# Performance work log

Measured on AMD Instinct MI355X. Metric: run time of the kernel, lower is better.

Reference implementation:

```python
import jax, jax.numpy as jnp
import numpy as np

IN_DIM = 8
MID = 128
HALF = IN_DIM // 2
N_BLOCKS = 8
B, H, W = 32, 96, 96


def _block_indices():
    # mask/inv_mask 1x1 convs are pure channel selections; precompute index form.
    half = HALF
    a1 = np.arange(half)              # first half channels
    a2 = np.arange(half, IN_DIM)      # second half channels
    b1 = 2 * np.arange(half)          # even channels
    b2 = 2 * np.arange(half) + 1      # odd channels
    # (change_idx, fix_idx) per block, matching self.masks = [(a1,a2),(a2,a1),(b1,b2),(b2,b1)]*2
    return [(a1, a2), (a2, a1), (b1, b2), (b2, b1)] * 2


def setup_inputs() -> dict:
    key = jax.random.key(0)
    ks = jax.random.split(key, 7)
    x = jax.random.normal(ks[0], (B, IN_DIM, H, W), dtype=jnp.float32)
    # stacked per-block 1x1-conv (pointwise) weights of the ST network
    W1 = jax.random.normal(ks[1], (N_BLOCKS, MID, HALF), dtype=jnp.float32) * 0.1
    b1 = jnp.zeros((N_BLOCKS, MID), dtype=jnp.float32)
    W2 = jax.random.normal(ks[2], (N_BLOCKS, MID, MID), dtype=jnp.float32) * 0.05
    b2 = jnp.zeros((N_BLOCKS, MID), dtype=jnp.float32)
    W3 = jax.random.normal(ks[3], (N_BLOCKS, 2 * HALF, MID), dtype=jnp.float32) * 0.05
    b3 = jnp.zeros((N_BLOCKS, 2 * HALF), dtype=jnp.float32)
    return {"x": x, "W1": W1, "b1": b1, "W2": W2, "b2": b2, "W3": W3, "b3": b3}


def _pw(h, w, b):
    # 1x1 conv == channel contraction
    return jnp.einsum('bchw,oc->bohw', h, w) + b[None, :, None, None]


def reference(x, W1, b1, W2, b2, W3, b3):
    pairs = _block_indices()
    log_det = jnp.zeros((x.shape[0], 1, x.shape[2], x.shape[3]), dtype=x.dtype)
    for i, (ci, fi) in enumerate(pairs):
        x_fix = x[:, fi]        # F.conv2d(x, inv_mask): channel gather
        x_change = x[:, ci]     # F.conv2d(x, mask): channel gather
        h = jax.nn.leaky_relu(_pw(x_fix, W1[i], b1[i]), 0.01)
        h = jax.nn.leaky_relu(_pw(h, W2[i], b2[i]), 0.01)
        st = jnp.tanh(_pw(h, W3[i], b3[i]))
        s, t = st[:, :HALF], st[:, HALF:]
        x_change = x_change * jnp.exp(s) + t
        # x*mask_nochange + conv(x_change, mask.T): replace changed channels in place
        x = x.at[:, ci].set(x_change)
        log_det = log_det + s.sum(axis=1, keepdims=True)
    return x, log_det
```

## Files before the change

### kernel.cpp

```cpp
#include <hip/hip_runtime.h>
#include <math.h>
#include <stdint.h>


#define HWPIX   9216
#define NPIX    294912
#define WSTRIDE 45056
#define NFRAG   45
#define L2OFF   4096
#define L3OFF   36864
#define B1OFF   40960
#define B2OFF   41472
#define B3OFF   41984

typedef float    f32x4 __attribute__((ext_vector_type(4)));
typedef _Float16 f16x4 __attribute__((ext_vector_type(4)));
typedef _Float16 f16x8 __attribute__((ext_vector_type(8)));
typedef uint32_t u32x4 __attribute__((ext_vector_type(4)));

__global__ __launch_bounds__(256)
void prep_frags(const float* __restrict__ W1, const float* __restrict__ b1,
                const float* __restrict__ W2, const float* __restrict__ b2,
                const float* __restrict__ W3, const float* __restrict__ b3,
                char* __restrict__ ws)
{
    int t = blockIdx.x * 256 + threadIdx.x;
    if (t >= 8 * NFRAG * 64) return;
    const int lane  = t & 63;
    const int f     = (t >> 6) % NFRAG;
    const int stage = t / (NFRAG * 64);
    const int pl = lane & 15, g = lane >> 4;
    const int pat = stage & 3;
    char* base = ws + stage * WSTRIDE;

    if (f < 8) {
        const int m = f;
        _Float16* dst = (_Float16*)(base + (m >> 1) * 1024 + lane * 16 + (m & 1) * 8);
#pragma unroll
        for (int e = 0; e < 4; ++e) {
            const int k = 4 * g + e;
            float val = 0.f;
            if (k < 8) {
                int j = -1;
                if      (pat == 0) j = (k >= 4) ? (k - 4) : -1;
                else if (pat == 1) j = (k < 4)  ? k        : -1;
                else if (pat == 2) j = (k & 1)  ? (k >> 1) : -1;
                else               j = (k & 1)  ? -1 : (k >> 1);
                if (j >= 0) val = W1[stage * 512 + (16 * m + pl) * 4 + j];
            }
            dst[e] = (_Float16)val;
        }
    } else if (f < 40) {
        const int idx = f - 8, m = idx >> 2, c = idx & 3;
        _Float16* dst = (_Float16*)(base + L2OFF + idx * 1024 + lane * 16);
#pragma unroll
        for (int e = 0; e < 8; ++e) {
            const int k32 = (e < 4) ? (4 * g + e) : (16 + 4 * g + (e - 4));
            dst[e] = (_Float16)W2[stage * 16384 + (16 * m + pl) * 128 + 32 * c + k32];
        }
    } else if (f < 44) {
        const int c = f - 40;
        _Float16* dst = (_Float16*)(base + L3OFF + c * 1024 + lane * 16);
#pragma unroll
        for (int e = 0; e < 8; ++e) {
            const int k32 = (e < 4) ? (4 * g + e) : (16 + 4 * g + (e - 4));
            dst[e] = (pl < 8) ? (_Float16)W3[stage * 1024 + pl * 128 + 32 * c + k32]
                              : (_Float16)0.f;
        }
    } else {
        float* d1 = (float*)(base + B1OFF);
        d1[2 * lane]     = b1[stage * 128 + 2 * lane];
        d1[2 * lane + 1] = b1[stage * 128 + 2 * lane + 1];
        float* d2 = (float*)(base + B2OFF);
        d2[2 * lane]     = b2[stage * 128 + 2 * lane];
        d2[2 * lane + 1] = b2[stage * 128 + 2 * lane + 1];
        if (lane < 16)
            ((float*)(base + B3OFF))[lane] = (lane < 8) ? b3[stage * 8 + lane] : 0.f;
    }
}

__device__ __forceinline__ void load_pair(const void* p, f16x4& a, f16x4& b) {
    f16x8 v = *(const f16x8*)p;
    a = __builtin_shufflevector(v, v, 0, 1, 2, 3);
    b = __builtin_shufflevector(v, v, 4, 5, 6, 7);
}

__device__ __forceinline__ f16x8 cat8(f16x4 a, f16x4 b) {
    return __builtin_shufflevector(a, b, 0, 1, 2, 3, 4, 5, 6, 7);
}

__device__ __forceinline__ f16x4 pack4(float a0, float a1, float a2, float a3) {
    auto lo = __builtin_amdgcn_cvt_pkrtz(a0, a1);
    auto hi = __builtin_amdgcn_cvt_pkrtz(a2, a3);
    f16x4 h;
    h[0] = (_Float16)lo[0]; h[1] = (_Float16)lo[1];
    h[2] = (_Float16)hi[0]; h[3] = (_Float16)hi[1];
    return h;
}

__device__ __forceinline__ f16x4 leaky_cvt(f32x4 a) {
    f16x4 h  = pack4(a[0], a[1], a[2], a[3]);
    f16x4 hs = h * (_Float16)0.01f;
    return __builtin_elementwise_max(h, hs);
}

__device__ __forceinline__ float fast_tanh(float x) {
    float e = __expf(2.0f * x);
    return 1.0f - 2.0f * __builtin_amdgcn_rcpf(e + 1.0f);
}

__global__ __launch_bounds__(256, 3)
void realnvp_mfma(const float* __restrict__ x_in,
                  const char* __restrict__ wfrag,
                  float* __restrict__ out)
{
    __shared__ __align__(16) char lds[WSTRIDE];

    const int tid  = threadIdx.x;
    const int w    = tid >> 6;
    const int lane = tid & 63;
    const int pl = lane & 15, g = lane >> 4;

    const int blockpx = blockIdx.x * 128;
    const int bb   = blockpx / HWPIX;
    const int rem0 = blockpx - bb * HWPIX + w * 32;
    const float* xb = x_in + (size_t)bb * 8 * HWPIX + rem0;

    float xv[2][4];
    float logdet[2] = {0.f, 0.f};
#pragma unroll
    for (int t = 0; t < 2; ++t)
#pragma unroll
        for (int e = 0; e < 4; ++e)
            xv[t][e] = (g < 2) ? xb[(size_t)(4 * g + e) * HWPIX + t * 16 + pl] : 0.f;

#pragma unroll 1
    for (int st = 0; st < 8; ++st) {
        __syncthreads();
        {
            const char* gsrc = wfrag + st * WSTRIDE + tid * 16;
            char*       ldst = lds + tid * 16;
#pragma unroll
            for (int it = 0; it < 11; ++it)
                *(u32x4*)(ldst + it * 4096) = *(const u32x4*)(gsrc + it * 4096);
        }
        __syncthreads();

        f16x4 xh[2];
#pragma unroll
        for (int t = 0; t < 2; ++t)
            xh[t] = pack4(xv[t][0], xv[t][1], xv[t][2], xv[t][3]);

        f16x4 h1[2][8];
        {
            f16x4 w1f[8];
#pragma unroll
            for (int pr = 0; pr < 4; ++pr)
                load_pair(lds + pr * 1024 + lane * 16, w1f[2 * pr], w1f[2 * pr + 1]);
#pragma unroll
            for (int m = 0; m < 8; ++m) {
                f32x4 bv = *(const f32x4*)(lds + B1OFF + m * 64 + g * 16);
#pragma unroll
                for (int t = 0; t < 2; ++t) {
                    f32x4 acc = __builtin_amdgcn_mfma_f32_16x16x16f16(w1f[m], xh[t], bv, 0, 0, 0);
                    h1[t][m] = leaky_cvt(acc);
                }
            }
        }

        f16x4 h2[2][8];
#pragma unroll
        for (int m = 0; m < 8; ++m) {
            f16x8 wf[4];
#pragma unroll
            for (int c = 0; c < 4; ++c)
                wf[c] = *(const f16x8*)(lds + L2OFF + (m * 4 + c) * 1024 + lane * 16);
            f32x4 bv = *(const f32x4*)(lds + B2OFF + m * 64 + g * 16);
#pragma unroll
            for (int t = 0; t < 2; ++t) {
                f32x4 acc = bv;
#pragma unroll
                for (int c = 0; c < 4; ++c)
                    acc = __builtin_amdgcn_mfma_f32_16x16x32_f16(
                        wf[c], cat8(h1[t][2 * c], h1[t][2 * c + 1]), acc, 0, 0, 0);
                h2[t][m] = leaky_cvt(acc);
            }
        }

        {
            f16x8 w3f[4];
#pragma unroll
            for (int c = 0; c < 4; ++c)
                w3f[c] = *(const f16x8*)(lds + L3OFF + c * 1024 + lane * 16);
            f32x4 bv3 = *(const f32x4*)(lds + B3OFF + g * 16);

            const int pat = st & 3;
#pragma unroll
            for (int t = 0; t < 2; ++t) {
                f32x4 acc = bv3;
#pragma unroll
                for (int c = 0; c < 4; ++c)
                    acc = __builtin_amdgcn_mfma_f32_16x16x32_f16(
                        w3f[c], cat8(h2[t][2 * c], h2[t][2 * c + 1]), acc, 0, 0, 0);

                float sv[4], ov[4];
#pragma unroll
                for (int r = 0; r < 4; ++r) sv[r] = fast_tanh(acc[r]);
#pragma unroll
                for (int r = 0; r < 4; ++r)
                    ov[r] = __int_as_float(
                        __builtin_amdgcn_ds_swizzle(__float_as_int(sv[r]), 0x401F));

                if (g == 0) logdet[t] += sv[0] + sv[1] + sv[2] + sv[3];

                float xn[4];
#pragma unroll
                for (int e = 0; e < 4; ++e) xn[e] = xv[t][e];
                if (pat == 0) {
#pragma unroll
                    for (int e = 0; e < 4; ++e)
                        if (g == 0) xn[e] = xv[t][e] * __expf(sv[e]) + ov[e];
                } else if (pat == 1) {
#pragma unroll
                    for (int e = 0; e < 4; ++e)
                        if (g == 1) xn[e] = xv[t][e] * __expf(ov[e]) + sv[e];
                } else if (pat == 2) {
#pragma unroll
                    for (int e = 0; e < 4; e += 2) {
                        const int k0 = e >> 1, k1 = 2 + (e >> 1);
                        if (g == 0) xn[e] = xv[t][e] * __expf(sv[k0]) + ov[k0];
                        if (g == 1) xn[e] = xv[t][e] * __expf(ov[k1]) + sv[k1];
                    }
                } else {
#pragma unroll
                    for (int e = 1; e < 4; e += 2) {
                        const int k0 = e >> 1, k1 = 2 + (e >> 1);
                        if (g == 0) xn[e] = xv[t][e] * __expf(sv[k0]) + ov[k0];
                        if (g == 1) xn[e] = xv[t][e] * __expf(ov[k1]) + sv[k1];
                    }
                }
#pragma unroll
                for (int e = 0; e < 4; ++e) xv[t][e] = xn[e];
            }
        }
    }

    float* outx = out + (size_t)bb * 8 * HWPIX + rem0;
#pragma unroll
    for (int t = 0; t < 2; ++t) {
        if (g < 2)
#pragma unroll
            for (int e = 0; e < 4; ++e)
                outx[(size_t)(4 * g + e) * HWPIX + t * 16 + pl] = xv[t][e];
        if (g == 0)
            out[(size_t)NPIX * 8 + (size_t)bb * HWPIX + rem0 + t * 16 + pl] = logdet[t];
    }
}

extern "C" void kernel_launch(void* const* d_in, const int* in_sizes, int n_in,
                              void* d_out, int out_size, void* d_ws, size_t ws_size,
                              hipStream_t stream)
{
    const float* x  = (const float*)d_in[0];
    const float* W1 = (const float*)d_in[1];
    const float* b1 = (const float*)d_in[2];
    const float* W2 = (const float*)d_in[3];
    const float* b2 = (const float*)d_in[4];
    const float* W3 = (const float*)d_in[5];
    const float* b3 = (const float*)d_in[6];
    float* out = (float*)d_out;
    char*  ws  = (char*)d_ws;

    hipLaunchKernelGGL(prep_frags, dim3(90), dim3(256), 0, stream,
                       W1, b1, W2, b2, W3, b3, ws);
    hipLaunchKernelGGL(realnvp_mfma, dim3(NPIX / 128), dim3(256), 0, stream,
                       x, ws, out);
}
```

Baseline: 175.6 us.

## Prefetch next stage weights into registers and shrink LDS for higher occupancy

Loads the next flow stage's weight fragments from global memory into registers while the current stage computes, then writes them to LDS after a barrier, so the global-load latency overlaps the MFMA work. Biases are now read straight from global memory rather than LDS, which shrinks the LDS buffer to 40 KB, and the launch bound is raised to 4 blocks per CU. The trade-off is 40 extra VGPRs held live across the compute phase, which together with the tighter occupancy target could cause register spills.

```diff
diff --git a/kernel.cpp b/kernel.cpp
--- a/kernel.cpp
+++ b/kernel.cpp
@@ -6,6 +6,7 @@
 #define HWPIX   9216
 #define NPIX    294912
 #define WSTRIDE 45056
+#define LDSBYTES 40960
 #define NFRAG   45
 #define L2OFF   4096
 #define L3OFF   36864
@@ -109,12 +110,12 @@
     return 1.0f - 2.0f * __builtin_amdgcn_rcpf(e + 1.0f);
 }
 
-__global__ __launch_bounds__(256, 3)
+__global__ __launch_bounds__(256, 4)
 void realnvp_mfma(const float* __restrict__ x_in,
                   const char* __restrict__ wfrag,
                   float* __restrict__ out)
 {
-    __shared__ __align__(16) char lds[WSTRIDE];
+    __shared__ __align__(16) char lds[LDSBYTES];
 
     const int tid  = threadIdx.x;
     const int w    = tid >> 6;
@@ -134,17 +135,25 @@
         for (int e = 0; e < 4; ++e)
             xv[t][e] = (g < 2) ? xb[(size_t)(4 * g + e) * HWPIX + t * 16 + pl] : 0.f;
 
+    u32x4 pf[10];
+#pragma unroll
+    for (int it = 0; it < 10; ++it)
+        pf[it] = *(const u32x4*)(wfrag + it * 4096 + tid * 16);
+#pragma unroll
+    for (int it = 0; it < 10; ++it)
+        *(u32x4*)(lds + it * 4096 + tid * 16) = pf[it];
+    __syncthreads();
+
 #pragma unroll 1
     for (int st = 0; st < 8; ++st) {
-        __syncthreads();
-        {
-            const char* gsrc = wfrag + st * WSTRIDE + tid * 16;
-            char*       ldst = lds + tid * 16;
-#pragma unroll
-            for (int it = 0; it < 11; ++it)
-                *(u32x4*)(ldst + it * 4096) = *(const u32x4*)(gsrc + it * 4096);
-        }
-        __syncthreads();
+        if (st < 7) {
+            const char* gsrc = wfrag + (st + 1) * WSTRIDE;
+#pragma unroll
+            for (int it = 0; it < 10; ++it)
+                pf[it] = *(const u32x4*)(gsrc + it * 4096 + tid * 16);
+        }
+
+        const char* bsrc = wfrag + st * WSTRIDE;
 
         f16x4 xh[2];
 #pragma unroll
@@ -159,7 +168,7 @@
                 load_pair(lds + pr * 1024 + lane * 16, w1f[2 * pr], w1f[2 * pr + 1]);
 #pragma unroll
             for (int m = 0; m < 8; ++m) {
-                f32x4 bv = *(const f32x4*)(lds + B1OFF + m * 64 + g * 16);
+                f32x4 bv = *(const f32x4*)(bsrc + B1OFF + m * 64 + g * 16);
 #pragma unroll
                 for (int t = 0; t < 2; ++t) {
                     f32x4 acc = __builtin_amdgcn_mfma_f32_16x16x16f16(w1f[m], xh[t], bv, 0, 0, 0);
@@ -175,7 +184,7 @@
 #pragma unroll
             for (int c = 0; c < 4; ++c)
                 wf[c] = *(const f16x8*)(lds + L2OFF + (m * 4 + c) * 1024 + lane * 16);
-            f32x4 bv = *(const f32x4*)(lds + B2OFF + m * 64 + g * 16);
+            f32x4 bv = *(const f32x4*)(bsrc + B2OFF + m * 64 + g * 16);
 #pragma unroll
             for (int t = 0; t < 2; ++t) {
                 f32x4 acc = bv;
@@ -192,7 +201,7 @@
 #pragma unroll
             for (int c = 0; c < 4; ++c)
                 w3f[c] = *(const f16x8*)(lds + L3OFF + c * 1024 + lane * 16);
-            f32x4 bv3 = *(const f32x4*)(lds + B3OFF + g * 16);
+            f32x4 bv3 = *(const f32x4*)(bsrc + B3OFF + g * 16);
 
             const int pat = st & 3;
 #pragma unroll
@@ -243,6 +252,14 @@
                 for (int e = 0; e < 4; ++e) xv[t][e] = xn[e];
             }
         }
+
+        __syncthreads();
+        if (st < 7) {
+#pragma unroll
+            for (int it = 0; it < 10; ++it)
+                *(u32x4*)(lds + it * 4096 + tid * 16) = pf[it];
+        }
+        __syncthreads();
     }
 
     float* outx = out + (size_t)bb * 8 * HWPIX + rem0;
```

Result: slower. 316.4 us (+80.1%).

## Process four pixel tiles per wave and read biases from global memory

Applied to the files above, without the earlier changes.

Each wave now handles 64 pixels (four 16-pixel tiles) instead of 32, so every block covers 256 pixels and the grid is halved. Each per-stage weight load into LDS and each weight-fragment read is reused across twice as many MFMAs. Biases are now read straight from global memory, which shrinks the LDS buffer and drops one copy iteration. The cost is higher register pressure from the doubled h1/h2 arrays, which may cause spills or lower occupancy under the 3-blocks launch bound, and fewer blocks to spread across the CUs.

```diff
diff --git a/kernel.cpp b/kernel.cpp
--- a/kernel.cpp
+++ b/kernel.cpp
@@ -12,6 +12,7 @@
 #define B1OFF   40960
 #define B2OFF   41472
 #define B3OFF   41984
+#define NT      4
 
 typedef float    f32x4 __attribute__((ext_vector_type(4)));
 typedef _Float16 f16x4 __attribute__((ext_vector_type(4)));
@@ -114,22 +115,22 @@
                   const char* __restrict__ wfrag,
                   float* __restrict__ out)
 {
-    __shared__ __align__(16) char lds[WSTRIDE];
+    __shared__ __align__(16) char lds[40960];
 
     const int tid  = threadIdx.x;
     const int w    = tid >> 6;
     const int lane = tid & 63;
     const int pl = lane & 15, g = lane >> 4;
 
-    const int blockpx = blockIdx.x * 128;
+    const int blockpx = blockIdx.x * 256;
     const int bb   = blockpx / HWPIX;
-    const int rem0 = blockpx - bb * HWPIX + w * 32;
+    const int rem0 = blockpx - bb * HWPIX + w * 64;
     const float* xb = x_in + (size_t)bb * 8 * HWPIX + rem0;
 
-    float xv[2][4];
-    float logdet[2] = {0.f, 0.f};
-#pragma unroll
-    for (int t = 0; t < 2; ++t)
+    float xv[NT][4];
+    float logdet[NT] = {0.f, 0.f, 0.f, 0.f};
+#pragma unroll
+    for (int t = 0; t < NT; ++t)
 #pragma unroll
         for (int e = 0; e < 4; ++e)
             xv[t][e] = (g < 2) ? xb[(size_t)(4 * g + e) * HWPIX + t * 16 + pl] : 0.f;
@@ -141,17 +142,19 @@
             const char* gsrc = wfrag + st * WSTRIDE + tid * 16;
             char*       ldst = lds + tid * 16;
 #pragma unroll
-            for (int it = 0; it < 11; ++it)
+            for (int it = 0; it < 10; ++it)
                 *(u32x4*)(ldst + it * 4096) = *(const u32x4*)(gsrc + it * 4096);
         }
         __syncthreads();
 
-        f16x4 xh[2];
-#pragma unroll
-        for (int t = 0; t < 2; ++t)
+        const char* wb = wfrag + st * WSTRIDE;
+
+        f16x4 xh[NT];
+#pragma unroll
+        for (int t = 0; t < NT; ++t)
             xh[t] = pack4(xv[t][0], xv[t][1], xv[t][2], xv[t][3]);
 
-        f16x4 h1[2][8];
+        f16x4 h1[NT][8];
         {
             f16x4 w1f[8];
 #pragma unroll
@@ -159,25 +162,25 @@
                 load_pair(lds + pr * 1024 + lane * 16, w1f[2 * pr], w1f[2 * pr + 1]);
 #pragma unroll
             for (int m = 0; m < 8; ++m) {
-                f32x4 bv = *(const f32x4*)(lds + B1OFF + m * 64 + g * 16);
-#pragma unroll
-                for (int t = 0; t < 2; ++t) {
+                f32x4 bv = *(const f32x4*)(wb + B1OFF + m * 64 + g * 16);
+#pragma unroll
+                for (int t = 0; t < NT; ++t) {
                     f32x4 acc = __builtin_amdgcn_mfma_f32_16x16x16f16(w1f[m], xh[t], bv, 0, 0, 0);
                     h1[t][m] = leaky_cvt(acc);
                 }
             }
         }
 
-        f16x4 h2[2][8];
+        f16x4 h2[NT][8];
 #pragma unroll
         for (int m = 0; m < 8; ++m) {
             f16x8 wf[4];
 #pragma unroll
             for (int c = 0; c < 4; ++c)
                 wf[c] = *(const f16x8*)(lds + L2OFF + (m * 4 + c) * 1024 + lane * 16);
-            f32x4 bv = *(const f32x4*)(lds + B2OFF + m * 64 + g * 16);
-#pragma unroll
-            for (int t = 0; t < 2; ++t) {
+            f32x4 bv = *(const f32x4*)(wb + B2OFF + m * 64 + g * 16);
+#pragma unroll
+            for (int t = 0; t < NT; ++t) {
                 f32x4 acc = bv;
 #pragma unroll
                 for (int c = 0; c < 4; ++c)
@@ -192,11 +195,11 @@
 #pragma unroll
             for (int c = 0; c < 4; ++c)
                 w3f[c] = *(const f16x8*)(lds + L3OFF + c * 1024 + lane * 16);
-            f32x4 bv3 = *(const f32x4*)(lds + B3OFF + g * 16);
+            f32x4 bv3 = *(const f32x4*)(wb + B3OFF + g * 16);
 
             const int pat = st & 3;
 #pragma unroll
-            for (int t = 0; t < 2; ++t) {
+            for (int t = 0; t < NT; ++t) {
                 f32x4 acc = bv3;
 #pragma unroll
                 for (int c = 0; c < 4; ++c)
@@ -247,7 +250,7 @@
 
     float* outx = out + (size_t)bb * 8 * HWPIX + rem0;
 #pragma unroll
-    for (int t = 0; t < 2; ++t) {
+    for (int t = 0; t < NT; ++t) {
         if (g < 2)
 #pragma unroll
             for (int e = 0; e < 4; ++e)
@@ -273,6 +276,6 @@
 
     hipLaunchKernelGGL(prep_frags, dim3(90), dim3(256), 0, stream,
                        W1, b1, W2, b2, W3, b3, ws);
-    hipLaunchKernelGGL(realnvp_mfma, dim3(NPIX / 128), dim3(256), 0, stream,
+    hipLaunchKernelGGL(realnvp_mfma, dim3(NPIX / 256), dim3(256), 0, stream,
                        x, ws, out);
 }
```

Measured after the change: 492.5 us. 2.8x slower.
